# Optimization experiments

Measured on AMD Instinct MI355X. Metric: run time of the kernel, lower is better.

## Reference

```python
import jax, jax.numpy as jnp
import numpy as np

B, H, W = 8, 56, 56
DIM, DIM_OUT, NUM_HEADS = 96, 192, 3
Q_STRIDE = (2, 2)


def setup_inputs() -> dict:
    key = jax.random.key(0)
    k1, k2, k3 = jax.random.split(key, 3)
    x = jax.random.normal(k1, (B, H, W, DIM), dtype=jnp.float32)
    W_qkv = jax.random.normal(k2, (DIM, 3 * DIM_OUT), dtype=jnp.float32) * 0.02
    b_qkv = jnp.zeros((3 * DIM_OUT,), dtype=jnp.float32)
    W_proj = jax.random.normal(k3, (DIM_OUT, DIM_OUT), dtype=jnp.float32) * 0.02
    b_proj = jnp.zeros((DIM_OUT,), dtype=jnp.float32)
    return {"x": x, "W_qkv": W_qkv, "b_qkv": b_qkv, "W_proj": W_proj, "b_proj": b_proj}


def reference(x, W_qkv, b_qkv, W_proj, b_proj):
    b, h, w, _ = x.shape
    c = W_proj.shape[0]          # dim_out
    nh = NUM_HEADS
    hd = c // nh                 # head_dim
    sh, sw = Q_STRIDE

    # fused QKV projection: (B,H,W,3*C)
    qkv = jnp.einsum("bhwd,de->bhwe", x, W_qkv) + b_qkv
    qkv = qkv.reshape(b, h * w, 3, nh, hd)
    q, k, v = qkv[:, :, 0], qkv[:, :, 1], qkv[:, :, 2]  # each (B,N,nh,hd)

    # query max-pool over spatial dims (channels = nh*hd, heads interleaved as in original)
    q = q.reshape(b, h, w, c)
    q = q.reshape(b, h // sh, sh, w // sw, sw, c).max(axis=(2, 4))  # (B,H',W',C)
    hn, wn = h // sh, w // sw
    q = q.reshape(b, hn * wn, nh, hd)

    # heads-first layout, scaled q
    q = q.transpose(0, 2, 1, 3) / jnp.sqrt(jnp.asarray(hd, x.dtype))  # (B,nh,Nq,hd)
    k = k.transpose(0, 2, 1, 3)                                       # (B,nh,Nk,hd)
    v = v.transpose(0, 2, 1, 3)

    attn = jax.nn.softmax(jnp.einsum("bnqd,bnkd->bnqk", q, k), axis=-1)
    out = jnp.einsum("bnqk,bnkd->bnqd", attn, v)        # (B,nh,Nq,hd)
    out = out.transpose(0, 2, 1, 3).reshape(b, hn, wn, c)

    return jnp.einsum("bhwc,cd->bhwd", out, W_proj) + b_proj
```

## Files before the change

kernel.cpp:

```cpp
#include <hip/hip_runtime.h>

#define BB    8
#define DIMO  192
#define NH    3
#define HD    64
#define NK    3136
#define NQ    784
#define M1    25088
#define M2    6272
#define KSPLIT 7
#define KSLICE 448
#define PSTR  56

typedef __bf16 bf16x8 __attribute__((ext_vector_type(8)));
typedef float f32x4  __attribute__((ext_vector_type(4)));

__device__ inline unsigned short f2bf(float f) {
    unsigned int u = __builtin_bit_cast(unsigned int, f);
    u += 0x7FFFu + ((u >> 16) & 1u);
    return (unsigned short)(u >> 16);
}

__global__ void wprep(const float* __restrict__ Wqkv, const float* __restrict__ Wproj,
                      unsigned short* __restrict__ Wb, unsigned short* __restrict__ Wpb) {
    __shared__ float Ls[192][33];
    const int t = threadIdx.x;
    if (blockIdx.x < 18) {
        const int n0 = blockIdx.x * 32;
        int rr = t >> 5, c = t & 31;
#pragma unroll
        for (int rb = 0; rb < 12; ++rb) {
            int row = rb * 8 + rr;
            Ls[row][c] = Wqkv[(size_t)row * 576 + n0 + c];
        }
        __syncthreads();
        int n = t >> 3, kc = (t & 7) * 12;
#pragma unroll
        for (int j = 0; j < 12; j += 4) {
            ushort4 u = { f2bf(Ls[kc + j][n]), f2bf(Ls[kc + j + 1][n]),
                          f2bf(Ls[kc + j + 2][n]), f2bf(Ls[kc + j + 3][n]) };
            *(ushort4*)(Wb + (size_t)(n0 + n) * 96 + kc + j) = u;
        }
    } else {
        const int n0 = (blockIdx.x - 18) * 32;
        int rr = t >> 5, c = t & 31;
#pragma unroll
        for (int rb = 0; rb < 24; ++rb) {
            int row = rb * 8 + rr;
            Ls[row][c] = Wproj[(size_t)row * 192 + n0 + c];
        }
        __syncthreads();
        int n = t >> 3, kc = (t & 7) * 24;
#pragma unroll
        for (int j = 0; j < 24; j += 4) {
            ushort4 u = { f2bf(Ls[kc + j][n]), f2bf(Ls[kc + j + 1][n]),
                          f2bf(Ls[kc + j + 2][n]), f2bf(Ls[kc + j + 3][n]) };
            *(ushort4*)(Wpb + (size_t)(n0 + n) * 192 + kc + j) = u;
        }
    }
}

__launch_bounds__(256)
__global__ void qkv_fused(const float* __restrict__ x,
                          const unsigned short* __restrict__ Wb,
                          const float* __restrict__ bias,
                          unsigned short* __restrict__ Qpb,
                          unsigned short* __restrict__ Kb,
                          unsigned short* __restrict__ Vt) {
    __shared__ __attribute__((aligned(16))) unsigned short xs[112 * 104];
    const int tid = threadIdx.x;
    const int wave = tid >> 6, lane = tid & 63;
    const int quad = lane >> 4, l16 = lane & 15;
    const int bid = blockIdx.x;

    if (bid < 784) {
        const int sec = (bid < 392) ? 1 : 2;
        const int m0 = ((bid < 392) ? bid : bid - 392) * 64;
#pragma unroll
        for (int i = 0; i < 6; ++i) {
            int f = tid + i * 256;
            int r = f / 24, c4 = f % 24;
            float4 v = ((const float4*)x)[(size_t)(m0 + r) * 24 + c4];
            ushort4 u = { f2bf(v.x), f2bf(v.y), f2bf(v.z), f2bf(v.w) };
            *(ushort4*)&xs[r * 104 + c4 * 4] = u;
        }
        __syncthreads();

        f32x4 acc[12];
#pragma unroll
        for (int i = 0; i < 12; ++i) acc[i] = (f32x4){0.f, 0.f, 0.f, 0.f};

        const unsigned short* wb = Wb + (size_t)(sec * 192 + l16) * 96 + quad * 8;
#pragma unroll
        for (int ch = 0; ch < 3; ++ch) {
            bf16x8 af = *(const bf16x8*)&xs[(wave * 16 + l16) * 104 + ch * 32 + quad * 8];
#pragma unroll
            for (int nf = 0; nf < 12; ++nf) {
                bf16x8 bfr = *(const bf16x8*)(wb + (size_t)nf * 16 * 96 + ch * 32);
                acc[nf] = __builtin_amdgcn_mfma_f32_16x16x32_bf16(af, bfr, acc[nf], 0, 0, 0);
            }
        }

        const int mbase = m0 + wave * 16 + quad * 4;
        if (sec == 1) {
#pragma unroll
            for (int nf = 0; nf < 12; ++nf) {
                int n = nf * 16 + l16;
                float bs = bias[192 + n];
#pragma unroll
                for (int i = 0; i < 4; ++i)
                    Kb[(size_t)(mbase + i) * 192 + n] = f2bf(acc[nf][i] + bs);
            }
        } else {
            int b = m0 / NK;
            int key = mbase - b * NK;
#pragma unroll
            for (int nf = 0; nf < 12; ++nf) {
                int n = nf * 16 + l16;
                float bs = bias[384 + n];
                int hh = n >> 6, dd = n & 63;
                ushort4 u = { f2bf(acc[nf][0] + bs), f2bf(acc[nf][1] + bs),
                              f2bf(acc[nf][2] + bs), f2bf(acc[nf][3] + bs) };
                *(ushort4*)(Vt + ((size_t)((b * 3 + hh) * 64 + dd)) * NK + key) = u;
            }
        }
    } else {
        const int t = bid - 784;
        const int b = t / 28, hq = t % 28;
        const int m0 = b * NK + hq * 112;
#pragma unroll
        for (int i = 0; i < 11; ++i) {
            int f = tid + i * 256;
            if (f < 2688) {
                int r = f / 24, c4 = f % 24;
                float4 v = ((const float4*)x)[(size_t)(m0 + r) * 24 + c4];
                int rp = 2 * (r % 56) + (r / 56);
                ushort4 u = { f2bf(v.x), f2bf(v.y), f2bf(v.z), f2bf(v.w) };
                *(ushort4*)&xs[rp * 104 + c4 * 4] = u;
            }
        }
        __syncthreads();

        f32x4 acc[7][3];
#pragma unroll
        for (int i = 0; i < 7; ++i)
#pragma unroll
            for (int j = 0; j < 3; ++j) acc[i][j] = (f32x4){0.f, 0.f, 0.f, 0.f};

        const unsigned short* wb = Wb + (size_t)(wave * 48 + l16) * 96 + quad * 8;
#pragma unroll
        for (int ch = 0; ch < 3; ++ch) {
            bf16x8 bfr[3];
#pragma unroll
            for (int jf = 0; jf < 3; ++jf)
                bfr[jf] = *(const bf16x8*)(wb + (size_t)jf * 16 * 96 + ch * 32);
#pragma unroll
            for (int mf = 0; mf < 7; ++mf) {
                bf16x8 a = *(const bf16x8*)&xs[(mf * 16 + l16) * 104 + ch * 32 + quad * 8];
#pragma unroll
                for (int jf = 0; jf < 3; ++jf)
                    acc[mf][jf] = __builtin_amdgcn_mfma_f32_16x16x32_bf16(a, bfr[jf], acc[mf][jf], 0, 0, 0);
            }
        }

#pragma unroll
        for (int mf = 0; mf < 7; ++mf) {
            int q = hq * 28 + mf * 4 + quad;
#pragma unroll
            for (int jf = 0; jf < 3; ++jf) {
                int n = wave * 48 + jf * 16 + l16;
                float m = fmaxf(fmaxf(acc[mf][jf][0], acc[mf][jf][1]),
                                fmaxf(acc[mf][jf][2], acc[mf][jf][3]));
                m = (m + bias[n]) * 0.125f;
                int hh = n >> 6, dd = n & 63;
                Qpb[((size_t)(b * 3 + hh) * NQ + q) * 64 + dd] = f2bf(m);
            }
        }
    }
}

__launch_bounds__(256)
__global__ void attn_mfma(const unsigned short* __restrict__ Qpb,
                          const unsigned short* __restrict__ Kb,
                          const unsigned short* __restrict__ Vt,
                          float* __restrict__ Pnum,
                          float* __restrict__ Pden) {
    __shared__ __attribute__((aligned(16))) unsigned short Ks[64 * 88];
    __shared__ __attribute__((aligned(16))) unsigned short Vs[64 * 88];
    __shared__ __attribute__((aligned(16))) unsigned short Ps[4 * 32 * PSTR];

    const int tid = threadIdx.x;
    const int wave = tid >> 6, lane = tid & 63;
    const int quad = lane >> 4, l16 = lane & 15;
    const int bh = blockIdx.y, b = bh / NH, h = bh % NH;
    const int qt = blockIdx.x * 128 + wave * 32;
    const int ks = blockIdx.z, k00 = ks * KSLICE;

    const int srow0 = tid >> 3, sch = (tid & 7) * 8;
    const unsigned short* kg  = Kb + ((size_t)(b * NK + k00) + srow0) * DIMO + h * 64 + sch;
    const unsigned short* kg1 = kg + (size_t)32 * DIMO;
    const unsigned short* vg  = Vt + ((size_t)bh * 64 + srow0) * NK + k00 + sch;
    const unsigned short* vg1 = vg + (size_t)32 * NK;

    uint4 kp0 = *(const uint4*)kg;
    uint4 kp1 = *(const uint4*)kg1;
    uint4 vp0 = *(const uint4*)vg;
    uint4 vp1 = *(const uint4*)vg1;

    int qa = min(qt + l16, NQ - 1);
    int qb = min(qt + 16 + l16, NQ - 1);
    const unsigned short* qpa = Qpb + ((size_t)bh * NQ + qa) * HD + quad * 8;
    const unsigned short* qpc = Qpb + ((size_t)bh * NQ + qb) * HD + quad * 8;
    bf16x8 qf[2][2];
    qf[0][0] = *(const bf16x8*)qpa;  qf[0][1] = *(const bf16x8*)(qpa + 32);
    qf[1][0] = *(const bf16x8*)qpc;  qf[1][1] = *(const bf16x8*)(qpc + 32);

    f32x4 on[4][2];
#pragma unroll
    for (int i = 0; i < 4; ++i)
#pragma unroll
        for (int j = 0; j < 2; ++j) on[i][j] = (f32x4){0.f, 0.f, 0.f, 0.f};
    float dden0 = 0.f, dden1 = 0.f;

    unsigned short* myP = Ps + wave * 32 * PSTR;

    for (int s = 0; s < 7; ++s) {
        __syncthreads();
        *(uint4*)&Ks[srow0 * 88 + sch]        = kp0;
        *(uint4*)&Ks[(srow0 + 32) * 88 + sch] = kp1;
        *(uint4*)&Vs[srow0 * 88 + sch]        = vp0;
        *(uint4*)&Vs[(srow0 + 32) * 88 + sch] = vp1;
        __syncthreads();
        if (s < 6) {
            kp0 = *(const uint4*)(kg  + (size_t)(s + 1) * 64 * DIMO);
            kp1 = *(const uint4*)(kg1 + (size_t)(s + 1) * 64 * DIMO);
            vp0 = *(const uint4*)(vg  + (s + 1) * 64);
            vp1 = *(const uint4*)(vg1 + (s + 1) * 64);
        }

#pragma unroll
        for (int half = 0; half < 2; ++half) {
#pragma unroll
            for (int ksub = 0; ksub < 2; ++ksub) {
                const int krow = (half * 32 + ksub * 16 + l16) * 88;
                bf16x8 kf0 = *(const bf16x8*)&Ks[krow + quad * 8];
                bf16x8 kf1 = *(const bf16x8*)&Ks[krow + 32 + quad * 8];
#pragma unroll
                for (int qsub = 0; qsub < 2; ++qsub) {
                    f32x4 sa = (f32x4){0.f, 0.f, 0.f, 0.f};
                    sa = __builtin_amdgcn_mfma_f32_16x16x32_bf16(kf0, qf[qsub][0], sa, 0, 0, 0);
                    sa = __builtin_amdgcn_mfma_f32_16x16x32_bf16(kf1, qf[qsub][1], sa, 0, 0, 0);
                    float p0 = __expf(sa[0]), p1 = __expf(sa[1]);
                    float p2 = __expf(sa[2]), p3 = __expf(sa[3]);
                    if (qsub == 0) dden0 += (p0 + p1) + (p2 + p3);
                    else           dden1 += (p0 + p1) + (p2 + p3);
                    ushort4 pw = { f2bf(p0), f2bf(p1), f2bf(p2), f2bf(p3) };
                    *(ushort4*)&myP[(qsub * 16 + l16) * PSTR + ksub * 16 + quad * 4] = pw;
                }
            }
            bf16x8 pf0 = *(const bf16x8*)&myP[l16 * PSTR + quad * 8];
            bf16x8 pf1 = *(const bf16x8*)&myP[(16 + l16) * PSTR + quad * 8];
#pragma unroll
            for (int dsub = 0; dsub < 4; ++dsub) {
                bf16x8 vf = *(const bf16x8*)&Vs[(dsub * 16 + l16) * 88 + half * 32 + quad * 8];
                on[dsub][0] = __builtin_amdgcn_mfma_f32_16x16x32_bf16(vf, pf0, on[dsub][0], 0, 0, 0);
                on[dsub][1] = __builtin_amdgcn_mfma_f32_16x16x32_bf16(vf, pf1, on[dsub][1], 0, 0, 0);
            }
        }
    }

#pragma unroll
    for (int qsub = 0; qsub < 2; ++qsub) {
        float r = (qsub == 0) ? dden0 : dden1;
        r += __shfl_xor(r, 16, 64);
        r += __shfl_xor(r, 32, 64);
        int q = qt + qsub * 16 + l16;
        if (q < NQ) {
            size_t base = (size_t)ks * (24 * NQ * HD) + ((size_t)bh * NQ + q) * HD + quad * 4;
#pragma unroll
            for (int dsub = 0; dsub < 4; ++dsub)
                *(f32x4*)(Pnum + base + dsub * 16) = on[dsub][qsub];
            if (quad == 0) Pden[ks * (24 * NQ) + bh * NQ + q] = r;
        }
    }
}

__launch_bounds__(256)
__global__ void proj_comb(const float* __restrict__ Pnum,
                          const float* __restrict__ Pden,
                          const unsigned short* __restrict__ Wpb,
                          const float* __restrict__ bproj,
                          float* __restrict__ out) {
    __shared__ __attribute__((aligned(16))) unsigned short as_[64 * 200];
    __shared__ float rden[64][4];
    const int tid = threadIdx.x;
    const int wave = tid >> 6, lane = tid & 63;
    const int quad = lane >> 4, l16 = lane & 15;
    const int m0 = blockIdx.x * 64;

    if (tid < 192) {
        int r = tid / 3, h = tid % 3;
        int gq = m0 + r, b = gq / NQ, qq = gq - b * NQ;
        float den = 0.f;
#pragma unroll
        for (int s = 0; s < KSPLIT; ++s)
            den += Pden[s * (24 * NQ) + (b * 3 + h) * NQ + qq];
        rden[r][h] = 1.0f / den;
    }
    __syncthreads();

    {
        int r = tid >> 2, cl = tid & 3;
        int gq = m0 + r, b = gq / NQ, qq = gq - b * NQ;
#pragma unroll
        for (int i = 0; i < 12; ++i) {
            int c = cl + i * 4;
            int h = c >> 4, d = (c & 15) * 4;
            const float* p = Pnum + ((size_t)(b * 3 + h) * NQ + qq) * 64 + d;
            f32x4 num = (f32x4){0.f, 0.f, 0.f, 0.f};
#pragma unroll
            for (int s = 0; s < KSPLIT; ++s)
                num = num + *(const f32x4*)(p + (size_t)s * (24 * NQ * HD));
            float rc = rden[r][h];
            ushort4 u = { f2bf(num[0] * rc), f2bf(num[1] * rc),
                          f2bf(num[2] * rc), f2bf(num[3] * rc) };
            *(ushort4*)&as_[r * 200 + c * 4] = u;
        }
    }
    __syncthreads();

    f32x4 acc[4][3];
#pragma unroll
    for (int i = 0; i < 4; ++i)
#pragma unroll
        for (int j = 0; j < 3; ++j) acc[i][j] = (f32x4){0.f, 0.f, 0.f, 0.f};

    const unsigned short* wp = Wpb + (size_t)(wave * 48 + l16) * 192 + quad * 8;
#pragma unroll
    for (int ch = 0; ch < 6; ++ch) {
        bf16x8 bfr[3];
#pragma unroll
        for (int jf = 0; jf < 3; ++jf)
            bfr[jf] = *(const bf16x8*)(wp + (size_t)jf * 16 * 192 + ch * 32);
#pragma unroll
        for (int mf = 0; mf < 4; ++mf) {
            bf16x8 a = *(const bf16x8*)&as_[(mf * 16 + l16) * 200 + ch * 32 + quad * 8];
#pragma unroll
            for (int jf = 0; jf < 3; ++jf)
                acc[mf][jf] = __builtin_amdgcn_mfma_f32_16x16x32_bf16(a, bfr[jf], acc[mf][jf], 0, 0, 0);
        }
    }

#pragma unroll
    for (int mf = 0; mf < 4; ++mf) {
        int m = m0 + mf * 16 + quad * 4;
#pragma unroll
        for (int jf = 0; jf < 3; ++jf) {
            int n = wave * 48 + jf * 16 + l16;
            float bs = bproj[n];
#pragma unroll
            for (int i = 0; i < 4; ++i)
                out[(size_t)(m + i) * 192 + n] = acc[mf][jf][i] + bs;
        }
    }
}

extern "C" void kernel_launch(void* const* d_in, const int* in_sizes, int n_in,
                              void* d_out, int out_size, void* d_ws, size_t ws_size,
                              hipStream_t stream) {
    const float* x     = (const float*)d_in[0];
    const float* Wqkv  = (const float*)d_in[1];
    const float* bqkv  = (const float*)d_in[2];
    const float* Wproj = (const float*)d_in[3];
    const float* bproj = (const float*)d_in[4];
    float* out = (float*)d_out;

    float* Pnum = (float*)d_ws;
    float* Pden = Pnum + (size_t)KSPLIT * 24 * NQ * HD;
    unsigned short* Qpb = (unsigned short*)(Pden + (size_t)KSPLIT * 24 * NQ);
    unsigned short* Kb  = Qpb + (size_t)24 * NQ * HD;
    unsigned short* Vt  = Kb + (size_t)BB * NK * DIMO;
    unsigned short* Wb  = Vt + (size_t)24 * HD * NK;
    unsigned short* Wpb = Wb + (size_t)576 * 96;

    wprep<<<24, 256, 0, stream>>>(Wqkv, Wproj, Wb, Wpb);

    qkv_fused<<<1008, 256, 0, stream>>>(x, Wb, bqkv, Qpb, Kb, Vt);

    attn_mfma<<<dim3(7, 24, KSPLIT), 256, 0, stream>>>(Qpb, Kb, Vt, Pnum, Pden);

    proj_comb<<<98, 256, 0, stream>>>(Pnum, Pden, Wpb, bproj, out);
}
```

Before: 134.3 us.

## Feed softmax probabilities to MFMA from registers and shrink projection tiles

In the attention kernel, the exponentiated scores are converted to bf16 and used directly as the B operand of a 16x16x16 bf16 MFMA, with no write to and read back from shared memory. This removes the LDS round-trip and the associated shared buffer, at the cost of twice as many smaller MFMA instructions for the PV product. The projection/combine kernel now processes 16 rows per block instead of 64, launching four times as many blocks to improve occupancy, at the cost of reloading the projection weights more often.

```diff
diff --git a/kernel.cpp b/kernel.cpp
--- a/kernel.cpp
+++ b/kernel.cpp
@@ -12,8 +12,15 @@
 #define KSLICE 448
 #define PSTR  56
 
+#if __has_builtin(__builtin_amdgcn_mfma_f32_16x16x16bf16_1k)
+#define HAVE_MFMA16 1
+#else
+#define HAVE_MFMA16 0
+#endif
+
 typedef __bf16 bf16x8 __attribute__((ext_vector_type(8)));
 typedef float f32x4  __attribute__((ext_vector_type(4)));
+typedef short s16x4  __attribute__((ext_vector_type(4)));
 
 __device__ inline unsigned short f2bf(float f) {
     unsigned int u = __builtin_bit_cast(unsigned int, f);
@@ -187,7 +194,9 @@
                           float* __restrict__ Pden) {
     __shared__ __attribute__((aligned(16))) unsigned short Ks[64 * 88];
     __shared__ __attribute__((aligned(16))) unsigned short Vs[64 * 88];
+#if !HAVE_MFMA16
     __shared__ __attribute__((aligned(16))) unsigned short Ps[4 * 32 * PSTR];
+#endif
 
     const int tid = threadIdx.x;
     const int wave = tid >> 6, lane = tid & 63;
@@ -222,7 +231,9 @@
         for (int j = 0; j < 2; ++j) on[i][j] = (f32x4){0.f, 0.f, 0.f, 0.f};
     float dden0 = 0.f, dden1 = 0.f;
 
+#if !HAVE_MFMA16
     unsigned short* myP = Ps + wave * 32 * PSTR;
+#endif
 
     for (int s = 0; s < 7; ++s) {
         __syncthreads();
@@ -238,6 +249,34 @@
             vp1 = *(const uint4*)(vg1 + (s + 1) * 64);
         }
 
+#if HAVE_MFMA16
+#pragma unroll
+        for (int g = 0; g < 4; ++g) {
+            const int krow = (g * 16 + l16) * 88;
+            bf16x8 kf0 = *(const bf16x8*)&Ks[krow + quad * 8];
+            bf16x8 kf1 = *(const bf16x8*)&Ks[krow + 32 + quad * 8];
+            s16x4 vf[4];
+#pragma unroll
+            for (int dsub = 0; dsub < 4; ++dsub)
+                vf[dsub] = *(const s16x4*)&Vs[(dsub * 16 + l16) * 88 + g * 16 + quad * 4];
+#pragma unroll
+            for (int qsub = 0; qsub < 2; ++qsub) {
+                f32x4 sa = (f32x4){0.f, 0.f, 0.f, 0.f};
+                sa = __builtin_amdgcn_mfma_f32_16x16x32_bf16(kf0, qf[qsub][0], sa, 0, 0, 0);
+                sa = __builtin_amdgcn_mfma_f32_16x16x32_bf16(kf1, qf[qsub][1], sa, 0, 0, 0);
+                float p0 = __expf(sa[0]), p1 = __expf(sa[1]);
+                float p2 = __expf(sa[2]), p3 = __expf(sa[3]);
+                if (qsub == 0) dden0 += (p0 + p1) + (p2 + p3);
+                else           dden1 += (p0 + p1) + (p2 + p3);
+                s16x4 pb = { (short)f2bf(p0), (short)f2bf(p1),
+                             (short)f2bf(p2), (short)f2bf(p3) };
+#pragma unroll
+                for (int dsub = 0; dsub < 4; ++dsub)
+                    on[dsub][qsub] = __builtin_amdgcn_mfma_f32_16x16x16bf16_1k(
+                        vf[dsub], pb, on[dsub][qsub], 0, 0, 0);
+            }
+        }
+#else
 #pragma unroll
         for (int half = 0; half < 2; ++half) {
 #pragma unroll
@@ -267,6 +306,7 @@
                 on[dsub][1] = __builtin_amdgcn_mfma_f32_16x16x32_bf16(vf, pf1, on[dsub][1], 0, 0, 0);
             }
         }
+#endif
     }
 
 #pragma unroll
@@ -291,14 +331,14 @@
                           const unsigned short* __restrict__ Wpb,
                           const float* __restrict__ bproj,
                           float* __restrict__ out) {
-    __shared__ __attribute__((aligned(16))) unsigned short as_[64 * 200];
-    __shared__ float rden[64][4];
+    __shared__ __attribute__((aligned(16))) unsigned short as_[16 * 200];
+    __shared__ float rden[16][4];
     const int tid = threadIdx.x;
     const int wave = tid >> 6, lane = tid & 63;
     const int quad = lane >> 4, l16 = lane & 15;
-    const int m0 = blockIdx.x * 64;
-
-    if (tid < 192) {
+    const int m0 = blockIdx.x * 16;
+
+    if (tid < 48) {
         int r = tid / 3, h = tid % 3;
         int gq = m0 + r, b = gq / NQ, qq = gq - b * NQ;
         float den = 0.f;
@@ -310,11 +350,11 @@
     __syncthreads();
 
     {
-        int r = tid >> 2, cl = tid & 3;
+        int r = tid >> 4, cl = tid & 15;
         int gq = m0 + r, b = gq / NQ, qq = gq - b * NQ;
 #pragma unroll
-        for (int i = 0; i < 12; ++i) {
-            int c = cl + i * 4;
+        for (int i = 0; i < 3; ++i) {
+            int c = cl + i * 16;
             int h = c >> 4, d = (c & 15) * 4;
             const float* p = Pnum + ((size_t)(b * 3 + h) * NQ + qq) * 64 + d;
             f32x4 num = (f32x4){0.f, 0.f, 0.f, 0.f};
@@ -329,39 +369,29 @@
     }
     __syncthreads();
 
-    f32x4 acc[4][3];
-#pragma unroll
-    for (int i = 0; i < 4; ++i)
-#pragma unroll
-        for (int j = 0; j < 3; ++j) acc[i][j] = (f32x4){0.f, 0.f, 0.f, 0.f};
+    f32x4 acc[3];
+#pragma unroll
+    for (int j = 0; j < 3; ++j) acc[j] = (f32x4){0.f, 0.f, 0.f, 0.f};
 
     const unsigned short* wp = Wpb + (size_t)(wave * 48 + l16) * 192 + quad * 8;
 #pragma unroll
     for (int ch = 0; ch < 6; ++ch) {
-        bf16x8 bfr[3];
-#pragma unroll
-        for (int jf = 0; jf < 3; ++jf)
-            bfr[jf] = *(const bf16x8*)(wp + (size_t)jf * 16 * 192 + ch * 32);
-#pragma unroll
-        for (int mf = 0; mf < 4; ++mf) {
-            bf16x8 a = *(const bf16x8*)&as_[(mf * 16 + l16) * 200 + ch * 32 + quad * 8];
-#pragma unroll
-            for (int jf = 0; jf < 3; ++jf)
-                acc[mf][jf] = __builtin_amdgcn_mfma_f32_16x16x32_bf16(a, bfr[jf], acc[mf][jf], 0, 0, 0);
-        }
-    }
-
-#pragma unroll
-    for (int mf = 0; mf < 4; ++mf) {
-        int m = m0 + mf * 16 + quad * 4;
+        bf16x8 a = *(const bf16x8*)&as_[l16 * 200 + ch * 32 + quad * 8];
 #pragma unroll
         for (int jf = 0; jf < 3; ++jf) {
-            int n = wave * 48 + jf * 16 + l16;
-            float bs = bproj[n];
-#pragma unroll
-            for (int i = 0; i < 4; ++i)
-                out[(size_t)(m + i) * 192 + n] = acc[mf][jf][i] + bs;
-        }
+            bf16x8 bfr = *(const bf16x8*)(wp + (size_t)jf * 16 * 192 + ch * 32);
+            acc[jf] = __builtin_amdgcn_mfma_f32_16x16x32_bf16(a, bfr, acc[jf], 0, 0, 0);
+        }
+    }
+
+    const int m = m0 + quad * 4;
+#pragma unroll
+    for (int jf = 0; jf < 3; ++jf) {
+        int n = wave * 48 + jf * 16 + l16;
+        float bs = bproj[n];
+#pragma unroll
+        for (int i = 0; i < 4; ++i)
+            out[(size_t)(m + i) * 192 + n] = acc[jf][i] + bs;
     }
 }
 
@@ -389,5 +419,5 @@
 
     attn_mfma<<<dim3(7, 24, KSPLIT), 256, 0, stream>>>(Qpb, Kb, Vt, Pnum, Pden);
 
-    proj_comb<<<98, 256, 0, stream>>>(Pnum, Pden, Wpb, bproj, out);
-}
+    proj_comb<<<392, 256, 0, stream>>>(Pnum, Pden, Wpb, bproj, out);
+}
```

After: 134.3 us. About the same (-0.0%).
